# Kernel tuning notes

Hardware: AMD Instinct MI355X
Metric: run time of the kernel (lower is better)

The kernel has to match this reference:

```python
import jax, jax.numpy as jnp
import numpy as np

B, T, C = 2, 2048, 2048
H, KV = 16, 4
D = C // H            # 128 head dim
G = H // KV           # 4 query heads per kv head
THETA = 10000.0


def setup_inputs() -> dict:
    key = jax.random.key(0)
    k0, k1, k2, k3 = jax.random.split(key, 4)
    s = 1.0 / np.sqrt(C)
    return {
        "x": jax.random.normal(k0, (B, T, C), jnp.float32),
        "Wq": jax.random.normal(k1, (H * D, C), jnp.float32) * s,
        "Wkv": jax.random.normal(k2, (2 * KV * D, C), jnp.float32) * s,
        "Wo": jax.random.normal(k3, (C, C), jnp.float32) * s,
    }


def _rotate_half(x):
    d = x.shape[-1] // 2
    return jnp.concatenate([-x[..., d:], x[..., :d]], axis=-1)


def _rope_tables(t, d):
    freqs = 1.0 / (THETA ** (jnp.arange(0, d, 2, dtype=jnp.float32) / d))
    ang = jnp.arange(t, dtype=jnp.float32)[:, None] * freqs[None, :]  # [T, d/2]
    emb = jnp.concatenate([ang, ang], axis=-1)                         # [T, d]
    return jnp.cos(emb), jnp.sin(emb)


def reference(x, Wq, Wkv, Wo):
    b, t, c = x.shape
    q = (x @ Wq.T).reshape(b, t, H, D).transpose(0, 2, 1, 3)      # [B,H,T,D]
    kv = (x @ Wkv.T).reshape(b, t, 2 * KV, D)
    k = kv[:, :, :KV].transpose(0, 2, 1, 3)                        # [B,KV,T,D]
    v = kv[:, :, KV:].transpose(0, 2, 1, 3)                        # [B,KV,T,D]

    cos, sin = _rope_tables(t, D)
    cos, sin = cos[None, None], sin[None, None]                    # [1,1,T,D]
    q = q * cos + _rotate_half(q) * sin
    k = k * cos + _rotate_half(k) * sin

    # GQA: keep k/v at KV heads; reshape q into [B,KV,G,T,D] instead of expanding k/v.
    qg = q.reshape(b, KV, G, t, D)
    scores = jnp.einsum('bkgtd,bksd->bkgts', qg, k) / jnp.sqrt(jnp.float32(D))
    causal = jnp.tril(jnp.ones((t, t), dtype=bool))                # is_causal=True path
    scores = jnp.where(causal, scores, -jnp.inf)
    p = jax.nn.softmax(scores, axis=-1)
    y = jnp.einsum('bkgts,bksd->bkgtd', p, v)                      # [B,KV,G,T,D]
    y = y.reshape(b, H, t, D).transpose(0, 2, 1, 3).reshape(b, t, c)
    return y @ Wo.T
```

## Files before the change

kernel.cpp:

```cpp
#include <hip/hip_runtime.h>

typedef unsigned short u16;
typedef __attribute__((ext_vector_type(4))) float f32x4;
typedef __attribute__((ext_vector_type(8))) __bf16 bf16x8;

__device__ __forceinline__ u16 f2bf(float f) {
    unsigned int x = __float_as_uint(f);
    x += 0x7fffu + ((x >> 16) & 1u);
    return (u16)(x >> 16);
}
__device__ __forceinline__ float bf2f(u16 u) {
    return __uint_as_float(((unsigned int)u) << 16);
}
__device__ __forceinline__ void async16(const void* g, void* l) {
    __builtin_amdgcn_global_load_lds(
        (const __attribute__((address_space(1))) void*)g,
        (__attribute__((address_space(3))) void*)l,
        16, 0, 0);
}

__global__ __launch_bounds__(256)
void cvt_all(const float* __restrict__ x,  const float* __restrict__ wq,
             const float* __restrict__ wkv, const float* __restrict__ wo,
             u16* __restrict__ xb, u16* __restrict__ wqb,
             u16* __restrict__ wkvb, u16* __restrict__ wob)
{
    const int nx = 8388608, nq = 4194304, nkv = 2097152;
    const int i = (blockIdx.x * 256 + threadIdx.x) * 4;
    const float* src; u16* dst; int off;
    if (i < nx)                 { src = x;   dst = xb;   off = i; }
    else if (i < nx + nq)       { src = wq;  dst = wqb;  off = i - nx; }
    else if (i < nx + nq + nkv) { src = wkv; dst = wkvb; off = i - nx - nq; }
    else                        { src = wo;  dst = wob;  off = i - nx - nq - nkv; }
    const float4 v = *(const float4*)(src + off);
    ushort4 o;
    o.x = f2bf(v.x); o.y = f2bf(v.y); o.z = f2bf(v.z); o.w = f2bf(v.w);
    *(ushort4*)(dst + off) = o;
}

template <int MODE>
__global__ __launch_bounds__(256)
void gemm_bt(const u16* __restrict__ A,
             const u16* __restrict__ B0,
             const u16* __restrict__ B1,
             u16* __restrict__ C,
             float* __restrict__ Cf,
             u16* __restrict__ vbuf,
             int M, int N, int K)
{
    __shared__ __align__(16) u16 As[128 * 32];
    __shared__ __align__(16) u16 Bs[128 * 32];

    const int tid  = threadIdx.x;
    const int w    = tid >> 6;
    const int lane = tid & 63;
    const int fl   = lane & 15;
    const int q4   = lane >> 4;
    const int m0   = blockIdx.y * 128;
    const int n0   = blockIdx.x * 128;
    const int wr   = w >> 1, wc = w & 1;

    const u16* Bp = B0;
    int nb = n0;
    if (MODE == 1 && n0 >= 2048) { Bp = B1; nb = n0 - 2048; }

    const int srow = lane >> 2;
    const int scol = (lane & 3) << 3;
    const u16* ag = A  + (size_t)(m0 + w * 32 + srow) * K + scol;
    const u16* bg = Bp + (size_t)(nb + w * 32 + srow) * K + scol;
    u16* al = &As[(w * 32) * 32];
    u16* bl = &Bs[(w * 32) * 32];

    f32x4 acc[4][4];
    for (int i = 0; i < 4; ++i)
        for (int j = 0; j < 4; ++j)
            acc[i][j] = f32x4{0.f, 0.f, 0.f, 0.f};

    for (int kt = 0; kt < K; kt += 32) {
        __syncthreads();
        async16(ag + kt,                    al);
        async16(ag + kt + (size_t)16 * K,   al + 16 * 32);
        async16(bg + kt,                    bl);
        async16(bg + kt + (size_t)16 * K,   bl + 16 * 32);
        __syncthreads();

        bf16x8 af[4], bfr[4];
        #pragma unroll
        for (int t = 0; t < 4; ++t) {
            af[t]  = *(const bf16x8*)&As[(wr * 64 + t * 16 + fl) * 32 + q4 * 8];
            bfr[t] = *(const bf16x8*)&Bs[(wc * 64 + t * 16 + fl) * 32 + q4 * 8];
        }
        #pragma unroll
        for (int mt = 0; mt < 4; ++mt)
            #pragma unroll
            for (int nt = 0; nt < 4; ++nt)
                acc[mt][nt] = __builtin_amdgcn_mfma_f32_16x16x32_bf16(
                    af[mt], bfr[nt], acc[mt][nt], 0, 0, 0);
    }

    #pragma unroll
    for (int mt = 0; mt < 4; ++mt) {
        #pragma unroll
        for (int nt = 0; nt < 4; ++nt) {
            const int colb = n0 + wc * 64 + nt * 16 + fl;
            #pragma unroll
            for (int r = 0; r < 4; ++r) {
                const int row = m0 + wr * 64 + mt * 16 + q4 * 4 + r;
                if (MODE == 0) {
                    Cf[(size_t)row * N + colb] = acc[mt][nt][r];
                } else {
                    const u16 val = f2bf(acc[mt][nt][r]);
                    if (colb < 2560) {
                        C[(size_t)row * 3072 + colb] = val;
                    } else {
                        const int f  = colb - 2560;
                        const int t  = row & 2047;
                        const int bb = row >> 11;
                        vbuf[((size_t)((bb << 2) + (f >> 7)) * 128 + (f & 127)) * 2048 + t] = val;
                    }
                }
            }
        }
    }
}

__global__ __launch_bounds__(256)
void rope_kernel(u16* __restrict__ qkv)
{
    const int idx = blockIdx.x * 256 + threadIdx.x;
    const int i   = idx & 63;
    const int t1  = idx >> 6;
    const int hh  = t1 % 20;
    const int m   = t1 / 20;
    const int pos = m & 2047;
    const bool isq = (hh < 16);
    const int col = isq ? (hh << 7) : (2048 + ((hh - 16) << 7));
    u16* p = qkv + (size_t)m * 3072 + col;

    const float inv = powf(10000.0f, -(float)(2 * i) * (1.0f / 128.0f));
    const float ang = (float)pos * inv;
    float s, c;
    sincosf(ang, &s, &c);
    const float sc = isq ? 0.08838834764831845f : 1.0f;
    const float x1 = bf2f(p[i]);
    const float x2 = bf2f(p[i + 64]);
    p[i]      = f2bf((x1 * c - x2 * s) * sc);
    p[i + 64] = f2bf((x2 * c + x1 * s) * sc);
}

__global__ __launch_bounds__(256, 2)
void attn_kernel(const u16* __restrict__ qkv,
                 const u16* __restrict__ vsrc,
                 u16* __restrict__ y)
{
    constexpr int T = 2048;
    const int lo  = blockIdx.x;
    const int hi  = 31 - lo;
    const int bh  = blockIdx.y;
    const int b   = bh >> 4;
    const int h   = bh & 15;
    const int kvh = h >> 2;

    const int tid  = threadIdx.x;
    const int w    = tid >> 6;
    const int lane = tid & 63;
    const int fl   = lane & 15;
    const int q4   = lane >> 4;

    __shared__ __align__(16) u16 Ks[2][64 * 128];
    __shared__ __align__(16) u16 Vt[2][128 * 64];
    __shared__ __align__(16) u16 Ps[64 * 72];

    const u16* Qg = qkv  + (size_t)(b * T) * 3072 + (h << 7);
    const u16* Kg = qkv  + (size_t)(b * T) * 3072 + 2048 + (kvh << 7);
    const u16* Vg = vsrc + (size_t)((b * 4 + kvh) * 128) * T;

    bf16x8 qf0[4], qf1[4];
    #pragma unroll
    for (int kc = 0; kc < 4; ++kc) {
        qf0[kc] = *(const bf16x8*)&Qg[(size_t)(lo * 64 + w * 16 + fl) * 3072 + kc * 32 + q4 * 8];
        qf1[kc] = *(const bf16x8*)&Qg[(size_t)(hi * 64 + w * 16 + fl) * 3072 + kc * 32 + q4 * 8];
    }

    int goffK[4], goffV[4], ldsC[4];
    #pragma unroll
    for (int i = 0; i < 4; ++i) {
        const int c  = w + 4 * i;
        const int rk = 4 * c + (lane >> 4);
        const int lk = (lane & 15) ^ (rk & 15);
        goffK[i] = rk * 3072 + lk * 8;
        const int rv = 8 * c + (lane >> 3);
        const int lv = (lane & 7) ^ ((lane >> 3) & 7);
        goffV[i] = rv * T + lv * 8;
        ldsC[i]  = c * 512;
    }

    #pragma unroll
    for (int i = 0; i < 4; ++i) {
        async16(Kg + goffK[i], &Ks[0][ldsC[i]]);
        async16(Vg + goffV[i], &Vt[0][ldsC[i]]);
    }

    float l0 = 0.f, l1 = 0.f;
    f32x4 o0[8], o1[8];
    #pragma unroll
    for (int dt = 0; dt < 8; ++dt) {
        o0[dt] = f32x4{0.f, 0.f, 0.f, 0.f};
        o1[dt] = f32x4{0.f, 0.f, 0.f, 0.f};
    }

    const int psrow = (w * 16 + fl) * 72;

    for (int j = 0; j <= hi; ++j) {
        __syncthreads();

        if (j < hi) {
            const u16* kb = Kg + (size_t)(j + 1) * 64 * 3072;
            const u16* vb = Vg + (j + 1) * 64;
            const int nb = (j + 1) & 1;
            #pragma unroll
            for (int i = 0; i < 4; ++i) {
                async16(kb + goffK[i], &Ks[nb][ldsC[i]]);
                async16(vb + goffV[i], &Vt[nb][ldsC[i]]);
            }
        }
        const int cb = j & 1;
        const bool dual = (j <= lo);

        f32x4 s0[4], s1[4];
        #pragma unroll
        for (int nt = 0; nt < 4; ++nt) {
            s0[nt] = f32x4{0.f, 0.f, 0.f, 0.f};
            s1[nt] = f32x4{0.f, 0.f, 0.f, 0.f};
        }
        if (dual) {
            #pragma unroll
            for (int kc = 0; kc < 4; ++kc)
                #pragma unroll
                for (int nt = 0; nt < 4; ++nt) {
                    bf16x8 aK = *(const bf16x8*)
                        &Ks[cb][(nt * 16 + fl) * 128 + (((kc << 2) + q4) ^ fl) * 8];
                    s1[nt] = __builtin_amdgcn_mfma_f32_16x16x32_bf16(aK, qf1[kc], s1[nt], 0, 0, 0);
                    s0[nt] = __builtin_amdgcn_mfma_f32_16x16x32_bf16(aK, qf0[kc], s0[nt], 0, 0, 0);
                }
        } else {
            #pragma unroll
            for (int kc = 0; kc < 4; ++kc)
                #pragma unroll
                for (int nt = 0; nt < 4; ++nt) {
                    bf16x8 aK = *(const bf16x8*)
                        &Ks[cb][(nt * 16 + fl) * 128 + (((kc << 2) + q4) ^ fl) * 8];
                    s1[nt] = __builtin_amdgcn_mfma_f32_16x16x32_bf16(aK, qf1[kc], s1[nt], 0, 0, 0);
                }
        }

        if (j == lo || j == hi) {
            const int qloc = w * 16 + fl;
            #pragma unroll
            for (int nt = 0; nt < 4; ++nt)
                #pragma unroll
                for (int r = 0; r < 4; ++r)
                    if (nt * 16 + q4 * 4 + r > qloc) {
                        if (j == lo) s0[nt][r] = -3e38f;
                        else         s1[nt][r] = -3e38f;
                    }
        }

        if (dual) {
            #pragma unroll
            for (int nt = 0; nt < 4; ++nt) {
                ushort4 pw;
                float p0 = __expf(s0[nt][0]);
                float p1 = __expf(s0[nt][1]);
                float p2 = __expf(s0[nt][2]);
                float p3 = __expf(s0[nt][3]);
                l0 += (p0 + p1) + (p2 + p3);
                pw.x = f2bf(p0); pw.y = f2bf(p1); pw.z = f2bf(p2); pw.w = f2bf(p3);
                *(ushort4*)&Ps[psrow + nt * 16 + q4 * 4] = pw;
            }
            asm volatile("s_waitcnt lgkmcnt(0)" ::: "memory");
            #pragma unroll
            for (int kc = 0; kc < 2; ++kc) {
                bf16x8 ap = *(const bf16x8*)&Ps[psrow + kc * 32 + q4 * 8];
                #pragma unroll
                for (int dt = 0; dt < 8; ++dt) {
                    bf16x8 bv = *(const bf16x8*)
                        &Vt[cb][(dt * 16 + fl) * 64 + (((kc << 2) + q4) ^ (fl & 7)) * 8];
                    o0[dt] = __builtin_amdgcn_mfma_f32_16x16x32_bf16(ap, bv, o0[dt], 0, 0, 0);
                }
            }
        }

        #pragma unroll
        for (int nt = 0; nt < 4; ++nt) {
            ushort4 pw;
            float p0 = __expf(s1[nt][0]);
            float p1 = __expf(s1[nt][1]);
            float p2 = __expf(s1[nt][2]);
            float p3 = __expf(s1[nt][3]);
            l1 += (p0 + p1) + (p2 + p3);
            pw.x = f2bf(p0); pw.y = f2bf(p1); pw.z = f2bf(p2); pw.w = f2bf(p3);
            *(ushort4*)&Ps[psrow + nt * 16 + q4 * 4] = pw;
        }
        asm volatile("s_waitcnt lgkmcnt(0)" ::: "memory");
        #pragma unroll
        for (int kc = 0; kc < 2; ++kc) {
            bf16x8 ap = *(const bf16x8*)&Ps[psrow + kc * 32 + q4 * 8];
            #pragma unroll
            for (int dt = 0; dt < 8; ++dt) {
                bf16x8 bv = *(const bf16x8*)
                    &Vt[cb][(dt * 16 + fl) * 64 + (((kc << 2) + q4) ^ (fl & 7)) * 8];
                o1[dt] = __builtin_amdgcn_mfma_f32_16x16x32_bf16(ap, bv, o1[dt], 0, 0, 0);
            }
        }
    }

    l0 += __shfl_xor(l0, 16, 64);
    l0 += __shfl_xor(l0, 32, 64);
    l1 += __shfl_xor(l1, 16, 64);
    l1 += __shfl_xor(l1, 32, 64);
    const float li0 = 1.0f / l0;
    const float li1 = 1.0f / l1;

    float lr0[4], lr1[4];
    #pragma unroll
    for (int r = 0; r < 4; ++r) {
        lr0[r] = __shfl(li0, q4 * 4 + r, 16);
        lr1[r] = __shfl(li1, q4 * 4 + r, 16);
    }
    #pragma unroll
    for (int dt = 0; dt < 8; ++dt)
        #pragma unroll
        for (int r = 0; r < 4; ++r) {
            const int row0 = lo * 64 + w * 16 + q4 * 4 + r;
            const int row1 = hi * 64 + w * 16 + q4 * 4 + r;
            y[(size_t)(b * T + row0) * 2048 + (h << 7) + dt * 16 + fl] =
                f2bf(o0[dt][r] * lr0[r]);
            y[(size_t)(b * T + row1) * 2048 + (h << 7) + dt * 16 + fl] =
                f2bf(o1[dt][r] * lr1[r]);
        }
}

extern "C" void kernel_launch(void* const* d_in, const int* in_sizes, int n_in,
                              void* d_out, int out_size, void* d_ws, size_t ws_size,
                              hipStream_t stream)
{
    const float* x   = (const float*)d_in[0];
    const float* Wq  = (const float*)d_in[1];
    const float* Wkv = (const float*)d_in[2];
    const float* Wo  = (const float*)d_in[3];
    float* out = (float*)d_out;

    const int nx = 4096 * 2048, nq = 2048 * 2048, nkv = 1024 * 2048, no = 2048 * 2048;

    u16* xb   = (u16*)d_ws;
    u16* wqb  = xb  + nx;
    u16* wkvb = wqb + nq;
    u16* wob  = wkvb + nkv;
    u16* qkv  = wob + no;
    u16* vbuf = qkv + (size_t)4096 * 3072;
    u16* y    = vbuf + (size_t)2 * 4 * 128 * 2048;

    const int ntot = nx + nq + nkv + no;
    cvt_all<<<ntot / 1024, 256, 0, stream>>>(x, Wq, Wkv, Wo, xb, wqb, wkvb, wob);

    dim3 g1(3072 / 128, 4096 / 128);
    gemm_bt<1><<<g1, 256, 0, stream>>>(xb, wqb, wkvb, qkv, nullptr, vbuf, 4096, 3072, 2048);

    rope_kernel<<<(4096 * 20 * 64) / 256, 256, 0, stream>>>(qkv);

    attn_kernel<<<dim3(16, 32), 256, 0, stream>>>(qkv, vbuf, y);

    dim3 g2(2048 / 128, 4096 / 128);
    gemm_bt<0><<<g2, 256, 0, stream>>>(y, wob, nullptr, nullptr, out, nullptr, 4096, 2048, 2048);
}
```

Measured before the change: 328.8 us.

## Rewrite projection GEMMs as 256x256 double-buffered, swizzled, XCD-remapped kernel

Replaces the 128x128 single-buffered GEMM with a 256x256 tile kernel of 512 threads and K-step 64. Global-to-LDS async loads are double-buffered and overlapped with MFMA work through explicit vmcnt waits and barriers. LDS columns are XOR-swizzled to avoid bank conflicts, and block IDs are remapped across the 8 XCDs for cache locality. It uses 128 KB of LDS per block and about 128 accumulator registers per thread. The smaller grid (192 and 128 blocks) may underfill 256 CUs.

```diff
diff --git a/kernel.cpp b/kernel.cpp
--- a/kernel.cpp
+++ b/kernel.cpp
@@ -17,6 +17,11 @@
         (const __attribute__((address_space(1))) void*)g,
         (__attribute__((address_space(3))) void*)l,
         16, 0, 0);
+}
+__device__ __forceinline__ void barrier_fence() {
+    asm volatile("" ::: "memory");
+    __builtin_amdgcn_s_barrier();
+    asm volatile("" ::: "memory");
 }
 
 __global__ __launch_bounds__(256)
@@ -39,8 +44,8 @@
 }
 
 template <int MODE>
-__global__ __launch_bounds__(256)
-void gemm_bt(const u16* __restrict__ A,
+__global__ __launch_bounds__(512, 2)
+void gemm256(const u16* __restrict__ A,
              const u16* __restrict__ B0,
              const u16* __restrict__ B1,
              u16* __restrict__ C,
@@ -48,64 +53,184 @@
              u16* __restrict__ vbuf,
              int M, int N, int K)
 {
-    __shared__ __align__(16) u16 As[128 * 32];
-    __shared__ __align__(16) u16 Bs[128 * 32];
+    __shared__ __align__(16) u16 As[32768];
+    __shared__ __align__(16) u16 Bs[32768];
 
     const int tid  = threadIdx.x;
     const int w    = tid >> 6;
     const int lane = tid & 63;
     const int fl   = lane & 15;
     const int q4   = lane >> 4;
-    const int m0   = blockIdx.y * 128;
-    const int n0   = blockIdx.x * 128;
-    const int wr   = w >> 1, wc = w & 1;
+    const int wm   = w >> 2;
+    const int wn   = w & 3;
+
+    const int gx  = gridDim.x;
+    const int nwg = gx * gridDim.y;
+    int id = blockIdx.y * gx + blockIdx.x;
+    const int cpx = nwg >> 3;
+    id = (id & 7) * cpx + (id >> 3);
+    const int m0 = (id / gx) * 256;
+    const int n0 = (id % gx) * 256;
 
     const u16* Bp = B0;
     int nb = n0;
     if (MODE == 1 && n0 >= 2048) { Bp = B1; nb = n0 - 2048; }
 
-    const int srow = lane >> 2;
-    const int scol = (lane & 3) << 3;
-    const u16* ag = A  + (size_t)(m0 + w * 32 + srow) * K + scol;
-    const u16* bg = Bp + (size_t)(nb + w * 32 + srow) * K + scol;
-    u16* al = &As[(w * 32) * 32];
-    u16* bl = &Bs[(w * 32) * 32];
-
-    f32x4 acc[4][4];
-    for (int i = 0; i < 4; ++i)
+    const int srow = w * 8 + (lane >> 3);
+    const int sg   = (lane & 7) ^ (lane >> 3);
+    const u16* agp = A  + (size_t)(m0 + srow) * K + sg * 8;
+    const u16* bgp = Bp + (size_t)(nb + srow) * K + sg * 8;
+    const int sbase = w * 512;
+
+    const int cswz    = (fl & 7) * 8;
+    const int colk0   = (q4 * 8) ^ cswz;
+    const int colk1   = (32 + q4 * 8) ^ cswz;
+    const int aBase   = wm * 8192 + fl * 64;
+    const int bBase   = (wn >> 1) * 8192 + ((wn & 1) * 64 + fl) * 64;
+
+    f32x4 acc[8][4];
+    #pragma unroll
+    for (int i = 0; i < 8; ++i)
+        #pragma unroll
         for (int j = 0; j < 4; ++j)
             acc[i][j] = f32x4{0.f, 0.f, 0.f, 0.f};
 
-    for (int kt = 0; kt < K; kt += 32) {
-        __syncthreads();
-        async16(ag + kt,                    al);
-        async16(ag + kt + (size_t)16 * K,   al + 16 * 32);
-        async16(bg + kt,                    bl);
-        async16(bg + kt + (size_t)16 * K,   bl + 16 * 32);
-        __syncthreads();
-
-        bf16x8 af[4], bfr[4];
-        #pragma unroll
-        for (int t = 0; t < 4; ++t) {
-            af[t]  = *(const bf16x8*)&As[(wr * 64 + t * 16 + fl) * 32 + q4 * 8];
-            bfr[t] = *(const bf16x8*)&Bs[(wc * 64 + t * 16 + fl) * 32 + q4 * 8];
-        }
+    bf16x8 aLo[4][2], aHi[4][2], bLo[2][2], bHi[2][2];
+
+    const int NT = K >> 6;
+
+    auto stage = [&](int t) {
+        const int tb = (t & 1) * 16384;
+        const size_t kof = (size_t)t * 64;
+        #pragma unroll
+        for (int h = 0; h < 2; ++h)
+            #pragma unroll
+            for (int rd = 0; rd < 2; ++rd) {
+                const size_t go = (size_t)(h * 128 + rd * 64) * K + kof;
+                const int lo = tb + h * 8192 + rd * 4096 + sbase;
+                async16(agp + go, &As[lo]);
+                async16(bgp + go, &Bs[lo]);
+            }
+    };
+    auto readALo = [&](int b) {
+        const int tb = b * 16384 + aBase;
+        #pragma unroll
+        for (int mt = 0; mt < 4; ++mt) {
+            aLo[mt][0] = *(const bf16x8*)&As[tb + mt * 1024 + colk0];
+            aLo[mt][1] = *(const bf16x8*)&As[tb + mt * 1024 + colk1];
+        }
+    };
+    auto readAHi = [&](int b) {
+        const int tb = b * 16384 + aBase;
+        #pragma unroll
+        for (int mt = 0; mt < 4; ++mt) {
+            aHi[mt][0] = *(const bf16x8*)&As[tb + (4 + mt) * 1024 + colk0];
+            aHi[mt][1] = *(const bf16x8*)&As[tb + (4 + mt) * 1024 + colk1];
+        }
+    };
+    auto readBLo = [&](int b) {
+        const int tb = b * 16384 + bBase;
+        #pragma unroll
+        for (int nt = 0; nt < 2; ++nt) {
+            bLo[nt][0] = *(const bf16x8*)&Bs[tb + nt * 1024 + colk0];
+            bLo[nt][1] = *(const bf16x8*)&Bs[tb + nt * 1024 + colk1];
+        }
+    };
+    auto readBHi = [&](int b) {
+        const int tb = b * 16384 + bBase;
+        #pragma unroll
+        for (int nt = 0; nt < 2; ++nt) {
+            bHi[nt][0] = *(const bf16x8*)&Bs[tb + (2 + nt) * 1024 + colk0];
+            bHi[nt][1] = *(const bf16x8*)&Bs[tb + (2 + nt) * 1024 + colk1];
+        }
+    };
+
+    stage(0);
+    stage(1);
+    asm volatile("s_waitcnt vmcnt(8)" ::: "memory");
+    barrier_fence();
+    readALo(0);
+    readBLo(0);
+
+    for (int t = 0; t < NT; ++t) {
+        const int b = t & 1;
+        readAHi(b);
+        barrier_fence();
+        __builtin_amdgcn_s_setprio(1);
         #pragma unroll
         for (int mt = 0; mt < 4; ++mt)
             #pragma unroll
-            for (int nt = 0; nt < 4; ++nt)
+            for (int nt = 0; nt < 2; ++nt) {
                 acc[mt][nt] = __builtin_amdgcn_mfma_f32_16x16x32_bf16(
-                    af[mt], bfr[nt], acc[mt][nt], 0, 0, 0);
-    }
-
-    #pragma unroll
-    for (int mt = 0; mt < 4; ++mt) {
+                    aLo[mt][0], bLo[nt][0], acc[mt][nt], 0, 0, 0);
+                acc[mt][nt] = __builtin_amdgcn_mfma_f32_16x16x32_bf16(
+                    aLo[mt][1], bLo[nt][1], acc[mt][nt], 0, 0, 0);
+            }
+        __builtin_amdgcn_s_setprio(0);
+        barrier_fence();
+
+        readBHi(b);
+        barrier_fence();
+        __builtin_amdgcn_s_setprio(1);
+        #pragma unroll
+        for (int mt = 0; mt < 4; ++mt)
+            #pragma unroll
+            for (int nt = 0; nt < 2; ++nt) {
+                acc[4 + mt][nt] = __builtin_amdgcn_mfma_f32_16x16x32_bf16(
+                    aHi[mt][0], bLo[nt][0], acc[4 + mt][nt], 0, 0, 0);
+                acc[4 + mt][nt] = __builtin_amdgcn_mfma_f32_16x16x32_bf16(
+                    aHi[mt][1], bLo[nt][1], acc[4 + mt][nt], 0, 0, 0);
+            }
+        __builtin_amdgcn_s_setprio(0);
+        barrier_fence();
+
+        __builtin_amdgcn_s_setprio(1);
+        #pragma unroll
+        for (int mt = 0; mt < 4; ++mt)
+            #pragma unroll
+            for (int nt = 0; nt < 2; ++nt) {
+                acc[4 + mt][2 + nt] = __builtin_amdgcn_mfma_f32_16x16x32_bf16(
+                    aHi[mt][0], bHi[nt][0], acc[4 + mt][2 + nt], 0, 0, 0);
+                acc[4 + mt][2 + nt] = __builtin_amdgcn_mfma_f32_16x16x32_bf16(
+                    aHi[mt][1], bHi[nt][1], acc[4 + mt][2 + nt], 0, 0, 0);
+            }
+        __builtin_amdgcn_s_setprio(0);
+        barrier_fence();
+
+        if (t + 2 < NT) {
+            stage(t + 2);
+            asm volatile("s_waitcnt vmcnt(8)" ::: "memory");
+        } else {
+            asm volatile("s_waitcnt vmcnt(0)" ::: "memory");
+        }
+        barrier_fence();
+
+        __builtin_amdgcn_s_setprio(1);
+        #pragma unroll
+        for (int mt = 0; mt < 4; ++mt)
+            #pragma unroll
+            for (int nt = 0; nt < 2; ++nt) {
+                acc[mt][2 + nt] = __builtin_amdgcn_mfma_f32_16x16x32_bf16(
+                    aLo[mt][0], bHi[nt][0], acc[mt][2 + nt], 0, 0, 0);
+                acc[mt][2 + nt] = __builtin_amdgcn_mfma_f32_16x16x32_bf16(
+                    aLo[mt][1], bHi[nt][1], acc[mt][2 + nt], 0, 0, 0);
+            }
+        __builtin_amdgcn_s_setprio(0);
+        if (t + 1 < NT) {
+            readALo(b ^ 1);
+            readBLo(b ^ 1);
+        }
+        barrier_fence();
+    }
+
+    #pragma unroll
+    for (int mt = 0; mt < 8; ++mt) {
         #pragma unroll
         for (int nt = 0; nt < 4; ++nt) {
-            const int colb = n0 + wc * 64 + nt * 16 + fl;
+            const int colb = n0 + wn * 64 + nt * 16 + fl;
             #pragma unroll
             for (int r = 0; r < 4; ++r) {
-                const int row = m0 + wr * 64 + mt * 16 + q4 * 4 + r;
+                const int row = m0 + wm * 128 + mt * 16 + q4 * 4 + r;
                 if (MODE == 0) {
                     Cf[(size_t)row * N + colb] = acc[mt][nt][r];
                 } else {
@@ -114,9 +239,9 @@
                         C[(size_t)row * 3072 + colb] = val;
                     } else {
                         const int f  = colb - 2560;
-                        const int t  = row & 2047;
+                        const int tt = row & 2047;
                         const int bb = row >> 11;
-                        vbuf[((size_t)((bb << 2) + (f >> 7)) * 128 + (f & 127)) * 2048 + t] = val;
+                        vbuf[((size_t)((bb << 2) + (f >> 7)) * 128 + (f & 127)) * 2048 + tt] = val;
                     }
                 }
             }
@@ -364,13 +489,13 @@
     const int ntot = nx + nq + nkv + no;
     cvt_all<<<ntot / 1024, 256, 0, stream>>>(x, Wq, Wkv, Wo, xb, wqb, wkvb, wob);
 
-    dim3 g1(3072 / 128, 4096 / 128);
-    gemm_bt<1><<<g1, 256, 0, stream>>>(xb, wqb, wkvb, qkv, nullptr, vbuf, 4096, 3072, 2048);
+    dim3 g1(3072 / 256, 4096 / 256);
+    gemm256<1><<<g1, 512, 0, stream>>>(xb, wqb, wkvb, qkv, nullptr, vbuf, 4096, 3072, 2048);
 
     rope_kernel<<<(4096 * 20 * 64) / 256, 256, 0, stream>>>(qkv);
 
     attn_kernel<<<dim3(16, 32), 256, 0, stream>>>(qkv, vbuf, y);
 
-    dim3 g2(2048 / 128, 4096 / 128);
-    gemm_bt<0><<<g2, 256, 0, stream>>>(y, wob, nullptr, nullptr, out, nullptr, 4096, 2048, 2048);
-}
+    dim3 g2(2048 / 256, 4096 / 256);
+    gemm256<0><<<g2, 512, 0, stream>>>(y, wob, nullptr, nullptr, out, nullptr, 4096, 2048, 2048);
+}
```

Measured after the change: 355.8 us. 1.08x slower.

## Replace GEMM with 256-row triple-buffered swizzled LDS pipeline and XCD-aware tile remap

Applied to the files above, without the earlier changes.

Both projection GEMMs move to a new kernel with 512 threads and 256-row tiles. It prefetches two K-tiles ahead through a three-slot LDS ring, using explicit vmcnt waits and a single barrier per step in place of two syncthreads per step. LDS columns are XOR-swizzled to cut bank conflicts, and block ids are remapped across XCDs for locality. MFMA sections are wrapped in raised wave priority. The aim is to hide global-load latency and increase reuse per tile, at the cost of more LDS and registers, which may lower occupancy.

```diff
diff --git a/kernel.cpp b/kernel.cpp
--- a/kernel.cpp
+++ b/kernel.cpp
@@ -17,6 +17,11 @@
         (const __attribute__((address_space(1))) void*)g,
         (__attribute__((address_space(3))) void*)l,
         16, 0, 0);
+}
+__device__ __forceinline__ void barrier_fence() {
+    asm volatile("" ::: "memory");
+    __builtin_amdgcn_s_barrier();
+    asm volatile("" ::: "memory");
 }
 
 __global__ __launch_bounds__(256)
@@ -38,74 +43,113 @@
     *(ushort4*)(dst + off) = o;
 }
 
-template <int MODE>
-__global__ __launch_bounds__(256)
-void gemm_bt(const u16* __restrict__ A,
-             const u16* __restrict__ B0,
-             const u16* __restrict__ B1,
-             u16* __restrict__ C,
-             float* __restrict__ Cf,
-             u16* __restrict__ vbuf,
-             int M, int N, int K)
+template <int MODE, int NTF>
+__global__ __launch_bounds__(512, 2)
+void gemm3buf(const u16* __restrict__ A,
+              const u16* __restrict__ B0,
+              const u16* __restrict__ B1,
+              u16* __restrict__ C,
+              float* __restrict__ Cf,
+              u16* __restrict__ vbuf,
+              int M, int N, int K)
 {
-    __shared__ __align__(16) u16 As[128 * 32];
-    __shared__ __align__(16) u16 Bs[128 * 32];
+    constexpr int BN  = NTF * 64;
+    constexpr int ASZ = 256 * 32;
+    constexpr int BSZ = BN * 32;
+    __shared__ __align__(16) u16 As[3 * ASZ];
+    __shared__ __align__(16) u16 Bs[3 * BSZ];
 
     const int tid  = threadIdx.x;
     const int w    = tid >> 6;
     const int lane = tid & 63;
     const int fl   = lane & 15;
     const int q4   = lane >> 4;
-    const int m0   = blockIdx.y * 128;
-    const int n0   = blockIdx.x * 128;
-    const int wr   = w >> 1, wc = w & 1;
+    const int wm   = w >> 2;
+    const int wn   = w & 3;
+
+    const int gx  = gridDim.x;
+    const int nwg = gx * gridDim.y;
+    int id = blockIdx.y * gx + blockIdx.x;
+    id = (id & 7) * (nwg >> 3) + (id >> 3);
+    const int m0 = (id / gx) * 256;
+    const int n0 = (id % gx) * BN;
 
     const u16* Bp = B0;
     int nb = n0;
     if (MODE == 1 && n0 >= 2048) { Bp = B1; nb = n0 - 2048; }
 
-    const int srow = lane >> 2;
-    const int scol = (lane & 3) << 3;
-    const u16* ag = A  + (size_t)(m0 + w * 32 + srow) * K + scol;
-    const u16* bg = Bp + (size_t)(nb + w * 32 + srow) * K + scol;
-    u16* al = &As[(w * 32) * 32];
-    u16* bl = &Bs[(w * 32) * 32];
-
-    f32x4 acc[4][4];
-    for (int i = 0; i < 4; ++i)
-        for (int j = 0; j < 4; ++j)
+    const int srow = w * 16 + (lane >> 2);
+    const int sg   = (lane & 3) ^ ((lane >> 3) & 3);
+    const u16* agp = A  + (size_t)(m0 + srow) * K + sg * 8;
+    const u16* bgp = Bp + (size_t)(nb + srow) * K + sg * 8;
+    const int aLds = (w * 16) * 32;
+    const int bLds = (w * 16) * 32;
+
+    const int cA = (q4 ^ ((fl >> 1) & 3)) * 8;
+
+    f32x4 acc[8][NTF];
+    #pragma unroll
+    for (int i = 0; i < 8; ++i)
+        #pragma unroll
+        for (int j = 0; j < NTF; ++j)
             acc[i][j] = f32x4{0.f, 0.f, 0.f, 0.f};
 
-    for (int kt = 0; kt < K; kt += 32) {
-        __syncthreads();
-        async16(ag + kt,                    al);
-        async16(ag + kt + (size_t)16 * K,   al + 16 * 32);
-        async16(bg + kt,                    bl);
-        async16(bg + kt + (size_t)16 * K,   bl + 16 * 32);
-        __syncthreads();
-
-        bf16x8 af[4], bfr[4];
-        #pragma unroll
-        for (int t = 0; t < 4; ++t) {
-            af[t]  = *(const bf16x8*)&As[(wr * 64 + t * 16 + fl) * 32 + q4 * 8];
-            bfr[t] = *(const bf16x8*)&Bs[(wc * 64 + t * 16 + fl) * 32 + q4 * 8];
-        }
-        #pragma unroll
-        for (int mt = 0; mt < 4; ++mt)
-            #pragma unroll
-            for (int nt = 0; nt < 4; ++nt)
+    const int NT = K >> 5;
+
+    auto stage = [&](int t, int bf) {
+        const size_t kof = (size_t)t * 32;
+        async16(agp + kof,                  &As[bf * ASZ + aLds]);
+        async16(agp + (size_t)128 * K + kof, &As[bf * ASZ + 128 * 32 + aLds]);
+        async16(bgp + kof,                  &Bs[bf * BSZ + bLds]);
+        if constexpr (NTF == 4)
+            async16(bgp + (size_t)128 * K + kof, &Bs[bf * BSZ + 128 * 32 + bLds]);
+    };
+
+    stage(0, 0);
+    stage(1, 1);
+
+    int bf = 0;
+    for (int t = 0; t < NT; ++t) {
+        if (t < NT - 1) {
+            if constexpr (NTF == 4) asm volatile("s_waitcnt vmcnt(4)" ::: "memory");
+            else                    asm volatile("s_waitcnt vmcnt(3)" ::: "memory");
+        } else {
+            asm volatile("s_waitcnt vmcnt(0)" ::: "memory");
+        }
+        barrier_fence();
+        const int bf2 = (bf + 2 >= 3) ? bf - 1 : bf + 2;
+        if (t + 2 < NT) stage(t + 2, bf2);
+
+        const int ab = bf * ASZ + wm * 4096 + fl * 32 + cA;
+        const int bb = bf * BSZ + wn * (NTF * 16) * 32 + fl * 32 + cA;
+        bf16x8 a[8], b[NTF];
+        #pragma unroll
+        for (int mt = 0; mt < 8; ++mt)
+            a[mt] = *(const bf16x8*)&As[ab + mt * 512];
+        #pragma unroll
+        for (int nt = 0; nt < NTF; ++nt)
+            b[nt] = *(const bf16x8*)&Bs[bb + nt * 512];
+
+        __builtin_amdgcn_s_setprio(1);
+        #pragma unroll
+        for (int mt = 0; mt < 8; ++mt)
+            #pragma unroll
+            for (int nt = 0; nt < NTF; ++nt)
                 acc[mt][nt] = __builtin_amdgcn_mfma_f32_16x16x32_bf16(
-                    af[mt], bfr[nt], acc[mt][nt], 0, 0, 0);
-    }
-
-    #pragma unroll
-    for (int mt = 0; mt < 4; ++mt) {
-        #pragma unroll
-        for (int nt = 0; nt < 4; ++nt) {
-            const int colb = n0 + wc * 64 + nt * 16 + fl;
+                    a[mt], b[nt], acc[mt][nt], 0, 0, 0);
+        __builtin_amdgcn_s_setprio(0);
+
+        bf = (bf + 1 >= 3) ? 0 : bf + 1;
+    }
+
+    #pragma unroll
+    for (int mt = 0; mt < 8; ++mt) {
+        #pragma unroll
+        for (int nt = 0; nt < NTF; ++nt) {
+            const int colb = n0 + wn * (NTF * 16) + nt * 16 + fl;
             #pragma unroll
             for (int r = 0; r < 4; ++r) {
-                const int row = m0 + wr * 64 + mt * 16 + q4 * 4 + r;
+                const int row = m0 + wm * 128 + mt * 16 + q4 * 4 + r;
                 if (MODE == 0) {
                     Cf[(size_t)row * N + colb] = acc[mt][nt][r];
                 } else {
@@ -114,9 +158,9 @@
                         C[(size_t)row * 3072 + colb] = val;
                     } else {
                         const int f  = colb - 2560;
-                        const int t  = row & 2047;
-                        const int bb = row >> 11;
-                        vbuf[((size_t)((bb << 2) + (f >> 7)) * 128 + (f & 127)) * 2048 + t] = val;
+                        const int tt = row & 2047;
+                        const int bb2 = row >> 11;
+                        vbuf[((size_t)((bb2 << 2) + (f >> 7)) * 128 + (f & 127)) * 2048 + tt] = val;
                     }
                 }
             }
@@ -364,13 +408,13 @@
     const int ntot = nx + nq + nkv + no;
     cvt_all<<<ntot / 1024, 256, 0, stream>>>(x, Wq, Wkv, Wo, xb, wqb, wkvb, wob);
 
-    dim3 g1(3072 / 128, 4096 / 128);
-    gemm_bt<1><<<g1, 256, 0, stream>>>(xb, wqb, wkvb, qkv, nullptr, vbuf, 4096, 3072, 2048);
+    dim3 g1(3072 / 256, 4096 / 256);
+    gemm3buf<1, 4><<<g1, 512, 0, stream>>>(xb, wqb, wkvb, qkv, nullptr, vbuf, 4096, 3072, 2048);
 
     rope_kernel<<<(4096 * 20 * 64) / 256, 256, 0, stream>>>(qkv);
 
     attn_kernel<<<dim3(16, 32), 256, 0, stream>>>(qkv, vbuf, y);
 
-    dim3 g2(2048 / 128, 4096 / 128);
-    gemm_bt<0><<<g2, 256, 0, stream>>>(y, wob, nullptr, nullptr, out, nullptr, 4096, 2048, 2048);
-}
+    dim3 g2(2048 / 128, 4096 / 256);
+    gemm3buf<0, 2><<<g2, 512, 0, stream>>>(y, wob, nullptr, nullptr, out, nullptr, 4096, 2048, 2048);
+}
```

Measured after the change: 356.1 us. +8.3%, slower.
